# Performance work log

Hardware: AMD Instinct MI355X
Metric: run time of the kernel (lower is better)

The kernel has to match this reference:

```python
import jax, jax.numpy as jnp
import numpy as np

N_IN = 3  # module default

def leaky_relu(x):
    return jnp.where(x > 0, x, 0.1 * x)  # LeakyReLU(alpha=0.1)

def setup_inputs() -> dict:
    key = jax.random.key(0)
    ks = jax.random.split(key, 6)
    B, N = 512, 16384
    inputs = jax.random.normal(ks[0], (B, N, 2 * N_IN), dtype=jnp.float32)
    # He-normal-ish small weights for the tiny 3-layer MLP (n_neurons=10, n_out-1=1)
    W1 = jax.random.normal(ks[1], (3, 10), dtype=jnp.float32) * jnp.sqrt(2.0 / 3)
    b1 = jnp.zeros((10,), jnp.float32)
    W2 = jax.random.normal(ks[2], (10, 10), dtype=jnp.float32) * jnp.sqrt(2.0 / 10)
    b2 = jnp.zeros((10,), jnp.float32)
    W3 = jax.random.normal(ks[3], (10, 10), dtype=jnp.float32) * jnp.sqrt(2.0 / 10)
    b3 = jnp.zeros((10,), jnp.float32)
    W4 = jax.random.normal(ks[4], (10, 1), dtype=jnp.float32) * jnp.sqrt(2.0 / 10)
    b4 = jnp.zeros((1,), jnp.float32)
    return {"inputs": inputs, "W1": W1, "b1": b1, "W2": W2, "b2": b2,
            "W3": W3, "b3": b3, "W4": W4, "b4": b4}

def reference(inputs, W1, b1, W2, b2, W3, b3, W4, b4):
    x = inputs
    # pairwise separation features (n_in = 3, positions at [0:3] and [3:6])
    sep_xy2 = jnp.square(x[..., N_IN + 1] - x[..., 1]) + jnp.square(x[..., N_IN] - x[..., 0])
    sep_z2 = jnp.square(x[..., N_IN + 2] - x[..., 2])
    sep_r2 = sep_xy2 + sep_z2                      # [B, N]
    dir_xy = (x[..., N_IN:N_IN + 2] - x[..., 0:2]) / sep_r2[..., None]  # [B, N, 2]
    # MLP input features: [z_i, z_j, sep_xy^2]
    Z = jnp.stack([x[..., 2], x[..., N_IN + 2], sep_xy2], axis=-1)      # [B, N, 3]
    # 3-layer MLP: LeakyReLU, tanh, LeakyReLU, then Dense(1)
    h = leaky_relu(Z @ W1 + b1)
    h = jnp.tanh(h @ W2 + b2)
    h = leaky_relu(h @ W3 + b3)
    F_amp = (h @ W4 + b4)[..., 0]                  # squeeze -> [B, N]
    # n_out == 2: broadcast amplitude over xy direction
    return F_amp[..., None] * dir_xy               # [B, N, 2]
```

## Files before the change

kernel.cpp:

```cpp
#include <hip/hip_runtime.h>


typedef float f32x4 __attribute__((ext_vector_type(4)));
typedef float f32x2 __attribute__((ext_vector_type(2)));

__device__ __forceinline__ f32x2 sp(float w) { return (f32x2){w, w}; }

__device__ __forceinline__ f32x2 fma2(f32x2 a, f32x2 b, f32x2 c) {
    return __builtin_elementwise_fma(a, b, c);
}

__device__ __forceinline__ f32x2 lrelu2(f32x2 x) {
    return __builtin_elementwise_max(x, x * 0.1f);
}

__device__ __forceinline__ float tanh_fast(float x) {
    float e = __expf(2.0f * x);
    return 1.0f - 2.0f * __builtin_amdgcn_rcpf(e + 1.0f);
}

__device__ __forceinline__ f32x2 tanh2(f32x2 a) {
    return (f32x2){tanh_fast(a[0]), tanh_fast(a[1])};
}

__global__ void __launch_bounds__(256) fused_mlp_kernel(
    const float* __restrict__ in,
    const float* __restrict__ W1, const float* __restrict__ b1,
    const float* __restrict__ W2, const float* __restrict__ b2,
    const float* __restrict__ W3, const float* __restrict__ b3,
    const float* __restrict__ W4, const float* __restrict__ b4,
    float* __restrict__ out, int npairs)
{
    int p = blockIdx.x * blockDim.x + threadIdx.x;
    if (p >= npairs) return;

    const f32x4* in4 = reinterpret_cast<const f32x4*>(in);
    f32x4 A = in4[3 * p + 0];
    f32x4 B = in4[3 * p + 1];
    f32x4 C = in4[3 * p + 2];

    f32x2 px0 = {A[0], B[2]}, py0 = {A[1], B[3]}, pz0 = {A[2], C[0]};
    f32x2 px1 = {A[3], C[1]}, py1 = {B[0], C[2]}, pz1 = {B[1], C[3]};

    f32x2 dx = px1 - px0;
    f32x2 dy = py1 - py0;
    f32x2 dz = pz1 - pz0;
    f32x2 sep_xy2 = fma2(dx, dx, dy * dy);
    f32x2 sep_r2  = fma2(dz, dz, sep_xy2);
    f32x2 inv_r2  = {__builtin_amdgcn_rcpf(sep_r2[0]),
                     __builtin_amdgcn_rcpf(sep_r2[1])};

    f32x2 Z0 = pz0;
    f32x2 Z1 = pz1;
    f32x2 Z2 = sep_xy2;

    f32x2 h1[10];
    #pragma unroll
    for (int j = 0; j < 10; ++j) {
        f32x2 a = sp(b1[j]);
        a = fma2(Z0, sp(W1[0 * 10 + j]), a);
        a = fma2(Z1, sp(W1[1 * 10 + j]), a);
        a = fma2(Z2, sp(W1[2 * 10 + j]), a);
        h1[j] = lrelu2(a);
    }

    f32x2 h2[10];
    #pragma unroll
    for (int j = 0; j < 10; ++j) {
        f32x2 a = sp(b2[j]);
        #pragma unroll
        for (int i = 0; i < 10; ++i) a = fma2(h1[i], sp(W2[i * 10 + j]), a);
        h2[j] = tanh2(a);
    }

    f32x2 h3[10];
    #pragma unroll
    for (int j = 0; j < 10; ++j) {
        f32x2 a = sp(b3[j]);
        #pragma unroll
        for (int i = 0; i < 10; ++i) a = fma2(h2[i], sp(W3[i * 10 + j]), a);
        h3[j] = lrelu2(a);
    }

    f32x2 f = sp(b4[0]);
    #pragma unroll
    for (int i = 0; i < 10; ++i) f = fma2(h3[i], sp(W4[i]), f);

    f32x2 s = f * inv_r2;
    f32x2 ox = s * dx;
    f32x2 oy = s * dy;

    f32x4 o;
    o[0] = ox[0]; o[1] = oy[0]; o[2] = ox[1]; o[3] = oy[1];
    reinterpret_cast<f32x4*>(out)[p] = o;
}

extern "C" void kernel_launch(void* const* d_in, const int* in_sizes, int n_in,
                              void* d_out, int out_size, void* d_ws, size_t ws_size,
                              hipStream_t stream) {
    const float* in = (const float*)d_in[0];
    const float* W1 = (const float*)d_in[1];
    const float* b1 = (const float*)d_in[2];
    const float* W2 = (const float*)d_in[3];
    const float* b2 = (const float*)d_in[4];
    const float* W3 = (const float*)d_in[5];
    const float* b3 = (const float*)d_in[6];
    const float* W4 = (const float*)d_in[7];
    const float* b4 = (const float*)d_in[8];
    float* out = (float*)d_out;

    int npairs = out_size / 4;
    int blocks = (npairs + 255) / 256;
    fused_mlp_kernel<<<blocks, 256, 0, stream>>>(
        in, W1, b1, W2, b2, W3, b3, W4, b4, out, npairs);
}
```

Before: 68.80 us.

## Pack MLP over neuron pairs with SGPR weight pairs via inline v_pk_fma op_sel

The kernel now vectorizes the MLP across pairs of output neurons within one sample, where it previously ran two samples side by side. Packed weight pairs are loaded as 64-bit scalar values and fed to inline-asm v_pk_fma_f32 with op_sel broadcasting one activation lane. This removes the per-FMA splat/broadcast of scalar weights into VGPRs and the duplicated weight handling. It also swaps expf for exp2 with a pre-scaled constant and an fma in tanh. The inline asm relies on the weight loads landing in SGPRs and on correct op_sel semantics, and the final dot product needs an extra horizontal add.

```diff
diff --git a/kernel.cpp b/kernel.cpp
--- a/kernel.cpp
+++ b/kernel.cpp
@@ -4,7 +4,17 @@
 typedef float f32x4 __attribute__((ext_vector_type(4)));
 typedef float f32x2 __attribute__((ext_vector_type(2)));
 
-__device__ __forceinline__ f32x2 sp(float w) { return (f32x2){w, w}; }
+__device__ __forceinline__ f32x2 fma2_splat(f32x2 a, int half, f32x2 w, f32x2 c) {
+    f32x2 d;
+    if (half == 0) {
+        asm("v_pk_fma_f32 %0, %1, %2, %3 op_sel:[0,0,0] op_sel_hi:[0,1,1]"
+            : "=v"(d) : "v"(a), "s"(w), "v"(c));
+    } else {
+        asm("v_pk_fma_f32 %0, %1, %2, %3 op_sel:[1,0,0] op_sel_hi:[1,1,1]"
+            : "=v"(d) : "v"(a), "s"(w), "v"(c));
+    }
+    return d;
+}
 
 __device__ __forceinline__ f32x2 fma2(f32x2 a, f32x2 b, f32x2 c) {
     return __builtin_elementwise_fma(a, b, c);
@@ -15,12 +25,12 @@
 }
 
 __device__ __forceinline__ float tanh_fast(float x) {
-    float e = __expf(2.0f * x);
-    return 1.0f - 2.0f * __builtin_amdgcn_rcpf(e + 1.0f);
+    float e = __builtin_amdgcn_exp2f(x * 2.8853900817779268f);
+    return fmaf(-2.0f, __builtin_amdgcn_rcpf(e + 1.0f), 1.0f);
 }
 
-__device__ __forceinline__ f32x2 tanh2(f32x2 a) {
-    return (f32x2){tanh_fast(a[0]), tanh_fast(a[1])};
+__device__ __forceinline__ f32x2 uld2(const float* __restrict__ p) {
+    return *reinterpret_cast<const f32x2*>(p);
 }
 
 __global__ void __launch_bounds__(256) fused_mlp_kernel(
@@ -39,59 +49,70 @@
     f32x4 B = in4[3 * p + 1];
     f32x4 C = in4[3 * p + 2];
 
-    f32x2 px0 = {A[0], B[2]}, py0 = {A[1], B[3]}, pz0 = {A[2], C[0]};
-    f32x2 px1 = {A[3], C[1]}, py1 = {B[0], C[2]}, pz1 = {B[1], C[3]};
+    float xs[2][6] = {
+        {A[0], A[1], A[2], A[3], B[0], B[1]},
+        {B[2], B[3], C[0], C[1], C[2], C[3]}
+    };
 
-    f32x2 dx = px1 - px0;
-    f32x2 dy = py1 - py0;
-    f32x2 dz = pz1 - pz0;
-    f32x2 sep_xy2 = fma2(dx, dx, dy * dy);
-    f32x2 sep_r2  = fma2(dz, dz, sep_xy2);
-    f32x2 inv_r2  = {__builtin_amdgcn_rcpf(sep_r2[0]),
-                     __builtin_amdgcn_rcpf(sep_r2[1])};
+    float oo[4];
 
-    f32x2 Z0 = pz0;
-    f32x2 Z1 = pz1;
-    f32x2 Z2 = sep_xy2;
+    #pragma unroll
+    for (int e = 0; e < 2; ++e) {
+        float dx = xs[e][3] - xs[e][0];
+        float dy = xs[e][4] - xs[e][1];
+        float dz = xs[e][5] - xs[e][2];
+        float sep_xy2 = fmaf(dx, dx, dy * dy);
+        float sep_r2  = fmaf(dz, dz, sep_xy2);
+        float inv_r2  = __builtin_amdgcn_rcpf(sep_r2);
 
-    f32x2 h1[10];
-    #pragma unroll
-    for (int j = 0; j < 10; ++j) {
-        f32x2 a = sp(b1[j]);
-        a = fma2(Z0, sp(W1[0 * 10 + j]), a);
-        a = fma2(Z1, sp(W1[1 * 10 + j]), a);
-        a = fma2(Z2, sp(W1[2 * 10 + j]), a);
-        h1[j] = lrelu2(a);
+        f32x2 zA; zA[0] = xs[e][2]; zA[1] = xs[e][5];
+        f32x2 zB; zB[0] = sep_xy2;  zB[1] = sep_xy2;
+
+        f32x2 h1p[5];
+        #pragma unroll
+        for (int jp = 0; jp < 5; ++jp) {
+            f32x2 a = fma2_splat(zA, 0, uld2(W1 + 0 * 10 + 2 * jp), uld2(b1 + 2 * jp));
+            a = fma2_splat(zA, 1, uld2(W1 + 1 * 10 + 2 * jp), a);
+            a = fma2_splat(zB, 0, uld2(W1 + 2 * 10 + 2 * jp), a);
+            h1p[jp] = lrelu2(a);
+        }
+
+        f32x2 h2p[5];
+        #pragma unroll
+        for (int jp = 0; jp < 5; ++jp) {
+            f32x2 a = fma2_splat(h1p[0], 0, uld2(W2 + 0 * 10 + 2 * jp), uld2(b2 + 2 * jp));
+            #pragma unroll
+            for (int i = 1; i < 10; ++i)
+                a = fma2_splat(h1p[i >> 1], i & 1, uld2(W2 + i * 10 + 2 * jp), a);
+            f32x2 t;
+            t[0] = tanh_fast(a[0]);
+            t[1] = tanh_fast(a[1]);
+            h2p[jp] = t;
+        }
+
+        f32x2 h3p[5];
+        #pragma unroll
+        for (int jp = 0; jp < 5; ++jp) {
+            f32x2 a = fma2_splat(h2p[0], 0, uld2(W3 + 0 * 10 + 2 * jp), uld2(b3 + 2 * jp));
+            #pragma unroll
+            for (int i = 1; i < 10; ++i)
+                a = fma2_splat(h2p[i >> 1], i & 1, uld2(W3 + i * 10 + 2 * jp), a);
+            h3p[jp] = lrelu2(a);
+        }
+
+        f32x2 fp = fma2(h3p[0], uld2(W4 + 0), (f32x2){b4[0], 0.0f});
+        #pragma unroll
+        for (int ip = 1; ip < 5; ++ip)
+            fp = fma2(h3p[ip], uld2(W4 + 2 * ip), fp);
+        float f = fp[0] + fp[1];
+
+        float s = f * inv_r2;
+        oo[2 * e + 0] = s * dx;
+        oo[2 * e + 1] = s * dy;
     }
 
-    f32x2 h2[10];
-    #pragma unroll
-    for (int j = 0; j < 10; ++j) {
-        f32x2 a = sp(b2[j]);
-        #pragma unroll
-        for (int i = 0; i < 10; ++i) a = fma2(h1[i], sp(W2[i * 10 + j]), a);
-        h2[j] = tanh2(a);
-    }
-
-    f32x2 h3[10];
-    #pragma unroll
-    for (int j = 0; j < 10; ++j) {
-        f32x2 a = sp(b3[j]);
-        #pragma unroll
-        for (int i = 0; i < 10; ++i) a = fma2(h2[i], sp(W3[i * 10 + j]), a);
-        h3[j] = lrelu2(a);
-    }
-
-    f32x2 f = sp(b4[0]);
-    #pragma unroll
-    for (int i = 0; i < 10; ++i) f = fma2(h3[i], sp(W4[i]), f);
-
-    f32x2 s = f * inv_r2;
-    f32x2 ox = s * dx;
-    f32x2 oy = s * dy;
-
     f32x4 o;
-    o[0] = ox[0]; o[1] = oy[0]; o[2] = ox[1]; o[3] = oy[1];
+    o[0] = oo[0]; o[1] = oo[1]; o[2] = oo[2]; o[3] = oo[3];
     reinterpret_cast<f32x4*>(out)[p] = o;
 }
 
```

Result: slower. 71.85 us (+4.4%).
